# Kernel optimization log

Hardware: AMD Instinct MI355X
Metric: run time of the kernel (lower is better)

Reference implementation:

```python
import jax, jax.numpy as jnp
import numpy as np

N = 32768      # total points (multiple of patch_size -> no padding needed)
C = 768        # channels
H = 8          # num heads
K = 256        # patch_size (window length)
HD = C // H    # head dim = 96, divisible by 6 (3 axes * rotary pairs)
FREQ = 100.0   # rope_freq


def rope3d(x, pos):
    """Point-position RoPE: head dim split into 3 axis chunks, each rotated
    by angles pos_axis * freq**(-i/half).  x: [N,H,HD], pos: [N,3] float."""
    d_axis = HD // 3            # 32
    half = d_axis // 2          # 16
    inv_freq = FREQ ** (-jnp.arange(half, dtype=x.dtype) / half)   # [half]
    ang = pos[:, :, None] * inv_freq[None, None, :]                # [N,3,half]
    cos = jnp.cos(ang)[:, None, :, :]                              # [N,1,3,half]
    sin = jnp.sin(ang)[:, None, :, :]
    xr = x.reshape(x.shape[0], x.shape[1], 3, d_axis)              # [N,H,3,d_axis]
    x1, x2 = xr[..., :half], xr[..., half:]
    out = jnp.concatenate([x1 * cos - x2 * sin, x1 * sin + x2 * cos], axis=-1)
    return out.reshape(x.shape)


def setup_inputs() -> dict:
    key = jax.random.key(0)
    ks = jax.random.split(key, 6)
    feat = jax.random.normal(ks[0], (N, C), dtype=jnp.float32)
    grid_coord = jax.random.randint(ks[1], (N, 3), 0, 1024, dtype=jnp.int32)
    order = jax.random.permutation(ks[2], N).astype(jnp.int32)     # serialized order
    inverse = jnp.argsort(order).astype(jnp.int32)                 # its inverse
    w_qkv = jax.random.normal(ks[3], (C, 3 * C), dtype=jnp.float32) * 0.02
    b_qkv = jnp.zeros((3 * C,), dtype=jnp.float32)
    w_proj = jax.random.normal(ks[4], (C, C), dtype=jnp.float32) * 0.02
    b_proj = jnp.zeros((C,), dtype=jnp.float32)
    return {"feat": feat, "grid_coord": grid_coord, "order": order,
            "inverse": inverse, "w_qkv": w_qkv, "b_qkv": b_qkv,
            "w_proj": w_proj, "b_proj": b_proj}


def reference(feat, grid_coord, order, inverse, w_qkv, b_qkv, w_proj, b_proj):
    scale = HD ** -0.5
    P = N // K  # number of windows
    qkv = (feat @ w_qkv + b_qkv)[order]                   # gather by serialized order
    pos = grid_coord[order].astype(feat.dtype)            # [N,3]
    q, k, v = jnp.split(qkv, 3, axis=-1)
    q = rope3d(q.reshape(N, H, HD), pos)
    k = rope3d(k.reshape(N, H, HD), pos)
    v = v.reshape(N, H, HD)
    # windowed (varlen with equal patch lengths) attention
    qw = q.reshape(P, K, H, HD)
    kw = k.reshape(P, K, H, HD)
    vw = v.reshape(P, K, H, HD)
    logits = jnp.einsum('pqhd,pkhd->phqk', qw, kw) * scale
    attn = jax.nn.softmax(logits, axis=-1)
    out = jnp.einsum('phqk,pkhd->pqhd', attn, vw).reshape(N, C)
    out = out[inverse]                                    # scatter back to input order
    return out @ w_proj + b_proj
```

## Files before the change

### kernel.cpp

```cpp
#include <hip/hip_runtime.h>
#include <hip/hip_bf16.h>
#include <stdint.h>

typedef __bf16 bf16_t;
typedef __bf16 bf16x8 __attribute__((ext_vector_type(8)));
typedef __bf16 bf16x4 __attribute__((ext_vector_type(4)));
typedef float f32x4 __attribute__((ext_vector_type(4)));

__device__ __forceinline__ void gload_lds16(const bf16_t* g, bf16_t* l) {
  __builtin_amdgcn_global_load_lds((const __attribute__((address_space(1))) void*)g,
                                   (__attribute__((address_space(3))) void*)l, 16, 0, 0);
}

__global__ __launch_bounds__(256) void transpose_cast_k(const float* __restrict__ W,
                                                        bf16_t* __restrict__ Bt,
                                                        int KDin, int MDin) {
  __shared__ float tile[64][65];
  const int bm = blockIdx.x, bk = blockIdx.y;
  const int c = threadIdx.x & 63, r0 = threadIdx.x >> 6;
#pragma unroll
  for (int rr = 0; rr < 16; ++rr) {
    int row = rr * 4 + r0;
    tile[row][c] = W[(size_t)(bk * 64 + row) * MDin + bm * 64 + c];
  }
  __syncthreads();
#pragma unroll
  for (int rr = 0; rr < 16; ++rr) {
    int mo = rr * 4 + r0;
    Bt[(size_t)(bm * 64 + mo) * KDin + bk * 64 + c] = (bf16_t)tile[c][mo];
  }
}

__global__ __launch_bounds__(256) void gather_cast_k(const float* __restrict__ feat,
                                                     const int* __restrict__ order,
                                                     bf16_t* __restrict__ featp) {
  const int id = blockIdx.x * 256 + threadIdx.x;
  const int j = id / 192;
  const int c = (id % 192) * 4;
  const int g = order[j];
  const float4 v = *(const float4*)(feat + (size_t)g * 768 + c);
  bf16x4 o;
  o[0] = (bf16_t)v.x; o[1] = (bf16_t)v.y; o[2] = (bf16_t)v.z; o[3] = (bf16_t)v.w;
  *(bf16x4*)(featp + (size_t)j * 768 + c) = o;
}

template <int MODE>
__global__ __launch_bounds__(256) void gemm_bt_k(const bf16_t* __restrict__ A,
                                                 const bf16_t* __restrict__ Bt,
                                                 const float* __restrict__ bias,
                                                 bf16_t* __restrict__ Cq,
                                                 bf16_t* __restrict__ Ck,
                                                 bf16_t* __restrict__ Cv,
                                                 float* __restrict__ Cf,
                                                 const int* __restrict__ order) {
  __shared__ bf16_t As[128 * 32];
  __shared__ bf16_t Bs[128 * 32];
  const int tid = threadIdx.x;
  const int lane = tid & 63;
  const int wave = tid >> 6;
  const int wr = wave >> 1, wc = wave & 1;
  const int lq = lane & 15, lk = lane >> 4;
  const int bx = blockIdx.x, by = blockIdx.y;

  const bf16_t* gA = A + (size_t)(by * 128 + (tid >> 2)) * 768 + (tid & 3) * 8;
  const bf16_t* gB = Bt + (size_t)(bx * 128 + (tid >> 2)) * 768 + (tid & 3) * 8;
  bf16_t* lA = As + tid * 8;
  bf16_t* lB = Bs + tid * 8;

  f32x4 acc[4][4] = {};

  for (int kk = 0; kk < 24; ++kk) {
    gload_lds16(gA, lA);
    gload_lds16(gA + 64 * 768, lA + 2048);
    gload_lds16(gB, lB);
    gload_lds16(gB + 64 * 768, lB + 2048);
    gA += 32;
    gB += 32;
    __syncthreads();
    bf16x8 af[4], bfr[4];
#pragma unroll
    for (int t = 0; t < 4; ++t) {
      af[t]  = *(const bf16x8*)(As + (wr * 64 + t * 16 + lq) * 32 + lk * 8);
      bfr[t] = *(const bf16x8*)(Bs + (wc * 64 + t * 16 + lq) * 32 + lk * 8);
    }
#pragma unroll
    for (int mt = 0; mt < 4; ++mt)
#pragma unroll
      for (int nt = 0; nt < 4; ++nt)
        acc[mt][nt] = __builtin_amdgcn_mfma_f32_16x16x32_bf16(af[mt], bfr[nt], acc[mt][nt], 0, 0, 0);
    __syncthreads();
  }

  const int colb = bx * 128 + wc * 64;
  float bcol[4];
#pragma unroll
  for (int nt = 0; nt < 4; ++nt) bcol[nt] = bias[colb + nt * 16 + lq];

#pragma unroll
  for (int mt = 0; mt < 4; ++mt) {
    const int row = by * 128 + wr * 64 + mt * 16 + lk * 4;
    if (MODE == 0) {
      bf16_t* base = (bx < 6) ? Cq : (bx < 12 ? Ck : Cv);
      const int coll = colb - (bx < 6 ? 0 : (bx < 12 ? 768 : 1536));
#pragma unroll
      for (int nt = 0; nt < 4; ++nt) {
        const int col = coll + nt * 16 + lq;
#pragma unroll
        for (int r = 0; r < 4; ++r)
          base[(size_t)(row + r) * 768 + col] = (bf16_t)(acc[mt][nt][r] + bcol[nt]);
      }
    } else {
      int ro[4];
#pragma unroll
      for (int r = 0; r < 4; ++r) ro[r] = order[row + r];
#pragma unroll
      for (int nt = 0; nt < 4; ++nt) {
        const int col = colb + nt * 16 + lq;
#pragma unroll
        for (int r = 0; r < 4; ++r)
          Cf[(size_t)ro[r] * 768 + col] = acc[mt][nt][r] + bcol[nt];
      }
    }
  }
}

__global__ __launch_bounds__(256) void rope_pack_k(bf16_t* __restrict__ Qb,
                                                   const bf16_t* __restrict__ Kb,
                                                   const bf16_t* __restrict__ Vb,
                                                   bf16_t* __restrict__ Kp,
                                                   bf16_t* __restrict__ Vp,
                                                   const int* __restrict__ grid_coord,
                                                   const int* __restrict__ order) {
  const int h = blockIdx.x, p = blockIdx.y;
  const int t = threadIdx.x;
  const int j = p * 256 + t;
  const int g = order[j];
  float pos[3];
  pos[0] = (float)grid_coord[g * 3 + 0];
  pos[1] = (float)grid_coord[g * 3 + 1];
  pos[2] = (float)grid_coord[g * 3 + 2];
  bf16_t* qrow = Qb + (size_t)j * 768 + h * 96;
  const bf16_t* krow = Kb + (size_t)j * 768 + h * 96;
  bf16_t* Kps = Kp + (size_t)(p * 8 + h) * 24576;
  const int nt = t >> 4, lqt = t & 15;
  const float NEGL = -0.41524101186f;
#pragma unroll
  for (int a = 0; a < 3; ++a) {
    const float pa = pos[a];
    bf16x8 q0 = *(bf16x8*)(qrow + a * 32);
    bf16x8 q1 = *(bf16x8*)(qrow + a * 32 + 8);
    bf16x8 q2 = *(bf16x8*)(qrow + a * 32 + 16);
    bf16x8 q3 = *(bf16x8*)(qrow + a * 32 + 24);
    bf16x8 k0 = *(const bf16x8*)(krow + a * 32);
    bf16x8 k1 = *(const bf16x8*)(krow + a * 32 + 8);
    bf16x8 k2 = *(const bf16x8*)(krow + a * 32 + 16);
    bf16x8 k3 = *(const bf16x8*)(krow + a * 32 + 24);
    float s[16], c[16];
#pragma unroll
    for (int i = 0; i < 16; ++i) {
      float ang = pa * exp2f(NEGL * (float)i);
      __sincosf(ang, &s[i], &c[i]);
    }
#pragma unroll
    for (int i = 0; i < 8; ++i) {
      float x1 = (float)q0[i], x2 = (float)q2[i];
      q0[i] = (bf16_t)(x1 * c[i] - x2 * s[i]);
      q2[i] = (bf16_t)(x1 * s[i] + x2 * c[i]);
      float y1 = (float)q1[i], y2 = (float)q3[i];
      q1[i] = (bf16_t)(y1 * c[i + 8] - y2 * s[i + 8]);
      q3[i] = (bf16_t)(y1 * s[i + 8] + y2 * c[i + 8]);
      float u1 = (float)k0[i], u2 = (float)k2[i];
      k0[i] = (bf16_t)(u1 * c[i] - u2 * s[i]);
      k2[i] = (bf16_t)(u1 * s[i] + u2 * c[i]);
      float w1 = (float)k1[i], w2 = (float)k3[i];
      k1[i] = (bf16_t)(w1 * c[i + 8] - w2 * s[i + 8]);
      k3[i] = (bf16_t)(w1 * s[i + 8] + w2 * c[i + 8]);
    }
    *(bf16x8*)(qrow + a * 32) = q0;
    *(bf16x8*)(qrow + a * 32 + 8) = q1;
    *(bf16x8*)(qrow + a * 32 + 16) = q2;
    *(bf16x8*)(qrow + a * 32 + 24) = q3;
    bf16_t* kf = Kps + (size_t)((nt * 3 + a) * 64 + lqt) * 8;
    *(bf16x8*)(kf)           = k0;
    *(bf16x8*)(kf + 16 * 8)  = k1;
    *(bf16x8*)(kf + 32 * 8)  = k2;
    *(bf16x8*)(kf + 48 * 8)  = k3;
  }
  const bf16_t* vrow = Vb + (size_t)j * 768 + h * 96;
  bf16_t* Vps = Vp + (size_t)(p * 8 + h) * 24576;
  const int kc8 = t >> 5, lkv = (t >> 3) & 3, jv = t & 7;
#pragma unroll
  for (int d0 = 0; d0 < 96; d0 += 8) {
    bf16x8 v = *(const bf16x8*)(vrow + d0);
    const int dt = d0 >> 4;
    bf16_t* vf = Vps + (size_t)((dt * 8 + kc8) * 64 + lkv * 16 + (d0 & 15)) * 8 + jv;
#pragma unroll
    for (int i = 0; i < 8; ++i) vf[i * 8] = v[i];
  }
}

__global__ __launch_bounds__(256) void attn_k(bf16_t* QO,
                                              const bf16_t* __restrict__ Kp,
                                              const bf16_t* __restrict__ Vp) {
  __shared__ bf16_t KV[24576];
  __shared__ bf16_t Pb[4][2048];
  const int bid = blockIdx.x;
  const int chunk = bid & 3;
  const int ph = bid >> 2;
  const int h = ph & 7, p = ph >> 3;
  const int tid = threadIdx.x, lane = tid & 63, wave = tid >> 6;
  const int lq = lane & 15, lk = lane >> 4;
  const int tok0 = p * 256;
  const int qrow0 = chunk * 64 + wave * 16;
  const bf16_t* Kps = Kp + (size_t)ph * 24576;
  const bf16_t* Vps = Vp + (size_t)ph * 24576;
  const float scale = 0.10206207262f;

#pragma unroll
  for (int i = 0; i < 12; ++i)
    gload_lds16(Kps + i * 2048 + tid * 8, KV + i * 2048 + tid * 8);
  bf16x8 aq[3];
  {
    const bf16_t* qb = QO + (size_t)(tok0 + qrow0 + lq) * 768 + h * 96 + lk * 8;
#pragma unroll
    for (int kc = 0; kc < 3; ++kc) aq[kc] = *(const bf16x8*)(qb + kc * 32);
  }
  __syncthreads();

  f32x4 sacc[16];
#pragma unroll
  for (int nt = 0; nt < 16; ++nt) {
    f32x4 acc = {0.f, 0.f, 0.f, 0.f};
#pragma unroll
    for (int kc = 0; kc < 3; ++kc) {
      bf16x8 bk = *(const bf16x8*)(KV + (size_t)((nt * 3 + kc) * 64 + lane) * 8);
      acc = __builtin_amdgcn_mfma_f32_16x16x32_bf16(aq[kc], bk, acc, 0, 0, 0);
    }
    sacc[nt] = acc;
  }
  __syncthreads();

#pragma unroll
  for (int i = 0; i < 12; ++i)
    gload_lds16(Vps + i * 2048 + tid * 8, KV + i * 2048 + tid * 8);

  float linv[4];
#pragma unroll
  for (int r = 0; r < 4; ++r) {
    float mx = -1e30f;
#pragma unroll
    for (int nt = 0; nt < 16; ++nt) mx = fmaxf(mx, sacc[nt][r]);
    mx = fmaxf(mx, __shfl_xor(mx, 1));
    mx = fmaxf(mx, __shfl_xor(mx, 2));
    mx = fmaxf(mx, __shfl_xor(mx, 4));
    mx = fmaxf(mx, __shfl_xor(mx, 8));
    mx *= scale;
    float l = 0.f;
#pragma unroll
    for (int nt = 0; nt < 16; ++nt) {
      float e = __expf(sacc[nt][r] * scale - mx);
      sacc[nt][r] = e;
      l += e;
    }
    l += __shfl_xor(l, 1);
    l += __shfl_xor(l, 2);
    l += __shfl_xor(l, 4);
    l += __shfl_xor(l, 8);
    linv[r] = 1.f / l;
  }
  __syncthreads();

  bf16_t* pw = &Pb[wave][0];
  f32x4 oacc[6] = {};
#pragma unroll
  for (int hf = 0; hf < 2; ++hf) {
#pragma unroll
    for (int ntl = 0; ntl < 8; ++ntl) {
      const int nt = hf * 8 + ntl;
      const int chk = ntl * 2 + (lq >> 3);
#pragma unroll
      for (int r = 0; r < 4; ++r) {
        const int row = lk * 4 + r;
        const int phys = chk ^ (row & 7);
        pw[row * 128 + phys * 8 + (lq & 7)] = (bf16_t)sacc[nt][r];
      }
    }
#pragma unroll
    for (int kcl = 0; kcl < 4; ++kcl) {
      const int physr = (kcl * 4 + lk) ^ (lq & 7);
      bf16x8 pf = *(const bf16x8*)(pw + lq * 128 + physr * 8);
      const int kc = hf * 4 + kcl;
#pragma unroll
      for (int dt = 0; dt < 6; ++dt) {
        bf16x8 vb = *(const bf16x8*)(KV + (size_t)((dt * 8 + kc) * 64 + lane) * 8);
        oacc[dt] = __builtin_amdgcn_mfma_f32_16x16x32_bf16(pf, vb, oacc[dt], 0, 0, 0);
      }
    }
  }

#pragma unroll
  for (int dt = 0; dt < 6; ++dt) {
#pragma unroll
    for (int r = 0; r < 4; ++r) {
      const int row = tok0 + qrow0 + lk * 4 + r;
      QO[(size_t)row * 768 + h * 96 + dt * 16 + lq] = (bf16_t)(oacc[dt][r] * linv[r]);
    }
  }
}

extern "C" void kernel_launch(void* const* d_in, const int* in_sizes, int n_in,
                              void* d_out, int out_size, void* d_ws, size_t ws_size,
                              hipStream_t stream) {
  const float* feat       = (const float*)d_in[0];
  const int*   grid_coord = (const int*)d_in[1];
  const int*   order      = (const int*)d_in[2];
  const float* w_qkv      = (const float*)d_in[4];
  const float* b_qkv      = (const float*)d_in[5];
  const float* w_proj     = (const float*)d_in[6];
  const float* b_proj     = (const float*)d_in[7];
  float* out = (float*)d_out;

  char* ws = (char*)d_ws;
  bf16_t* Bt1   = (bf16_t*)(ws);
  bf16_t* Bt2   = (bf16_t*)(ws + 3538944);
  bf16_t* featp = (bf16_t*)(ws + 4718592);
  bf16_t* Kp    = featp;
  bf16_t* Qb    = (bf16_t*)(ws + 55050240);
  bf16_t* Kb    = (bf16_t*)(ws + 105381888);
  bf16_t* Vb    = (bf16_t*)(ws + 155713536);
  bf16_t* Vp    = (bf16_t*)(ws + 206045184);

  transpose_cast_k<<<dim3(36, 12), 256, 0, stream>>>(w_qkv, Bt1, 768, 2304);
  transpose_cast_k<<<dim3(12, 12), 256, 0, stream>>>(w_proj, Bt2, 768, 768);
  gather_cast_k<<<24576, 256, 0, stream>>>(feat, order, featp);
  gemm_bt_k<0><<<dim3(18, 256), 256, 0, stream>>>(featp, Bt1, b_qkv, Qb, Kb, Vb, nullptr, nullptr);
  rope_pack_k<<<dim3(8, 128), 256, 0, stream>>>(Qb, Kb, Vb, Kp, Vp, grid_coord, order);
  attn_k<<<4096, 256, 0, stream>>>(Qb, Kp, Vp);
  gemm_bt_k<1><<<dim3(6, 256), 256, 0, stream>>>(Qb, Bt2, b_proj, nullptr, nullptr, nullptr, out, order);
}
```

Before: 560.6 us.

## Fuse RoPE into QKV GEMM epilogue and stage V transpose through LDS

Gathered positions are precomputed once in the gather kernel, and RoPE is applied to Q and K inside the QKV GEMM epilogue in fp32 before the bf16 store. This removes the separate read-modify-write of Q and the per-thread sincos recomputation. The pack kernel now only relayouts K with coalesced 16-byte copies and transposes V through padded shared memory, replacing scattered 2-byte global stores. posf shares its workspace with Vp; this is safe only because posf is consumed by the GEMM before pack_k writes Vp. Rounding also shifts slightly, since RoPE is now applied before the bf16 cast rather than after.

```diff
diff --git a/kernel.cpp b/kernel.cpp
--- a/kernel.cpp
+++ b/kernel.cpp
@@ -33,7 +33,9 @@
 
 __global__ __launch_bounds__(256) void gather_cast_k(const float* __restrict__ feat,
                                                      const int* __restrict__ order,
-                                                     bf16_t* __restrict__ featp) {
+                                                     const int* __restrict__ grid_coord,
+                                                     bf16_t* __restrict__ featp,
+                                                     float* __restrict__ posf) {
   const int id = blockIdx.x * 256 + threadIdx.x;
   const int j = id / 192;
   const int c = (id % 192) * 4;
@@ -42,6 +44,11 @@
   bf16x4 o;
   o[0] = (bf16_t)v.x; o[1] = (bf16_t)v.y; o[2] = (bf16_t)v.z; o[3] = (bf16_t)v.w;
   *(bf16x4*)(featp + (size_t)j * 768 + c) = o;
+  if (c == 0) {
+    posf[j * 3 + 0] = (float)grid_coord[g * 3 + 0];
+    posf[j * 3 + 1] = (float)grid_coord[g * 3 + 1];
+    posf[j * 3 + 2] = (float)grid_coord[g * 3 + 2];
+  }
 }
 
 template <int MODE>
@@ -52,7 +59,8 @@
                                                  bf16_t* __restrict__ Ck,
                                                  bf16_t* __restrict__ Cv,
                                                  float* __restrict__ Cf,
-                                                 const int* __restrict__ order) {
+                                                 const int* __restrict__ order,
+                                                 const float* __restrict__ posf) {
   __shared__ bf16_t As[128 * 32];
   __shared__ bf16_t Bs[128 * 32];
   const int tid = threadIdx.x;
@@ -96,23 +104,57 @@
 #pragma unroll
   for (int nt = 0; nt < 4; ++nt) bcol[nt] = bias[colb + nt * 16 + lq];
 
-#pragma unroll
-  for (int mt = 0; mt < 4; ++mt) {
-    const int row = by * 128 + wr * 64 + mt * 16 + lk * 4;
-    if (MODE == 0) {
-      bf16_t* base = (bx < 6) ? Cq : (bx < 12 ? Ck : Cv);
-      const int coll = colb - (bx < 6 ? 0 : (bx < 12 ? 768 : 1536));
-#pragma unroll
-      for (int nt = 0; nt < 4; ++nt) {
-        const int col = coll + nt * 16 + lq;
-#pragma unroll
-        for (int r = 0; r < 4; ++r)
-          base[(size_t)(row + r) * 768 + col] = (bf16_t)(acc[mt][nt][r] + bcol[nt]);
+  if (MODE == 0) {
+    bf16_t* base = (bx < 6) ? Cq : (bx < 12 ? Ck : Cv);
+    const int coll = colb - (bx < 6 ? 0 : (bx < 12 ? 768 : 1536));
+    if (bx < 12) {
+      const int a0 = (colb % 96) >> 5;
+      const int a1 = ((colb + 32) % 96) >> 5;
+      const float fr = exp2f(-0.41524101186f * (float)lq);
+#pragma unroll
+      for (int mt = 0; mt < 4; ++mt) {
+        const int rowb = by * 128 + wr * 64 + mt * 16 + lk * 4;
+#pragma unroll
+        for (int r = 0; r < 4; ++r) {
+          const int row = rowb + r;
+          float s0, c0, s1, c1;
+          __sincosf(posf[row * 3 + a0] * fr, &s0, &c0);
+          __sincosf(posf[row * 3 + a1] * fr, &s1, &c1);
+          const float x1 = acc[mt][0][r] + bcol[0], x2 = acc[mt][1][r] + bcol[1];
+          const float y1 = acc[mt][2][r] + bcol[2], y2 = acc[mt][3][r] + bcol[3];
+          acc[mt][0][r] = x1 * c0 - x2 * s0;
+          acc[mt][1][r] = x1 * s0 + x2 * c0;
+          acc[mt][2][r] = y1 * c1 - y2 * s1;
+          acc[mt][3][r] = y1 * s1 + y2 * c1;
+        }
+#pragma unroll
+        for (int nt = 0; nt < 4; ++nt) {
+          const int col = coll + nt * 16 + lq;
+#pragma unroll
+          for (int r = 0; r < 4; ++r)
+            base[(size_t)(rowb + r) * 768 + col] = (bf16_t)acc[mt][nt][r];
+        }
       }
     } else {
+#pragma unroll
+      for (int mt = 0; mt < 4; ++mt) {
+        const int rowb = by * 128 + wr * 64 + mt * 16 + lk * 4;
+#pragma unroll
+        for (int nt = 0; nt < 4; ++nt) {
+          const int col = coll + nt * 16 + lq;
+#pragma unroll
+          for (int r = 0; r < 4; ++r)
+            base[(size_t)(rowb + r) * 768 + col] = (bf16_t)(acc[mt][nt][r] + bcol[nt]);
+        }
+      }
+    }
+  } else {
+#pragma unroll
+    for (int mt = 0; mt < 4; ++mt) {
+      const int rowb = by * 128 + wr * 64 + mt * 16 + lk * 4;
       int ro[4];
 #pragma unroll
-      for (int r = 0; r < 4; ++r) ro[r] = order[row + r];
+      for (int r = 0; r < 4; ++r) ro[r] = order[rowb + r];
 #pragma unroll
       for (int nt = 0; nt < 4; ++nt) {
         const int col = colb + nt * 16 + lq;
@@ -124,78 +166,43 @@
   }
 }
 
-__global__ __launch_bounds__(256) void rope_pack_k(bf16_t* __restrict__ Qb,
-                                                   const bf16_t* __restrict__ Kb,
-                                                   const bf16_t* __restrict__ Vb,
-                                                   bf16_t* __restrict__ Kp,
-                                                   bf16_t* __restrict__ Vp,
-                                                   const int* __restrict__ grid_coord,
-                                                   const int* __restrict__ order) {
+__global__ __launch_bounds__(256) void pack_k(const bf16_t* __restrict__ Kb,
+                                              const bf16_t* __restrict__ Vb,
+                                              bf16_t* __restrict__ Kp,
+                                              bf16_t* __restrict__ Vp) {
+  __shared__ bf16_t VT[96 * 264];
   const int h = blockIdx.x, p = blockIdx.y;
-  const int t = threadIdx.x;
-  const int j = p * 256 + t;
-  const int g = order[j];
-  float pos[3];
-  pos[0] = (float)grid_coord[g * 3 + 0];
-  pos[1] = (float)grid_coord[g * 3 + 1];
-  pos[2] = (float)grid_coord[g * 3 + 2];
-  bf16_t* qrow = Qb + (size_t)j * 768 + h * 96;
-  const bf16_t* krow = Kb + (size_t)j * 768 + h * 96;
-  bf16_t* Kps = Kp + (size_t)(p * 8 + h) * 24576;
-  const int nt = t >> 4, lqt = t & 15;
-  const float NEGL = -0.41524101186f;
-#pragma unroll
-  for (int a = 0; a < 3; ++a) {
-    const float pa = pos[a];
-    bf16x8 q0 = *(bf16x8*)(qrow + a * 32);
-    bf16x8 q1 = *(bf16x8*)(qrow + a * 32 + 8);
-    bf16x8 q2 = *(bf16x8*)(qrow + a * 32 + 16);
-    bf16x8 q3 = *(bf16x8*)(qrow + a * 32 + 24);
-    bf16x8 k0 = *(const bf16x8*)(krow + a * 32);
-    bf16x8 k1 = *(const bf16x8*)(krow + a * 32 + 8);
-    bf16x8 k2 = *(const bf16x8*)(krow + a * 32 + 16);
-    bf16x8 k3 = *(const bf16x8*)(krow + a * 32 + 24);
-    float s[16], c[16];
-#pragma unroll
-    for (int i = 0; i < 16; ++i) {
-      float ang = pa * exp2f(NEGL * (float)i);
-      __sincosf(ang, &s[i], &c[i]);
-    }
-#pragma unroll
-    for (int i = 0; i < 8; ++i) {
-      float x1 = (float)q0[i], x2 = (float)q2[i];
-      q0[i] = (bf16_t)(x1 * c[i] - x2 * s[i]);
-      q2[i] = (bf16_t)(x1 * s[i] + x2 * c[i]);
-      float y1 = (float)q1[i], y2 = (float)q3[i];
-      q1[i] = (bf16_t)(y1 * c[i + 8] - y2 * s[i + 8]);
-      q3[i] = (bf16_t)(y1 * s[i + 8] + y2 * c[i + 8]);
-      float u1 = (float)k0[i], u2 = (float)k2[i];
-      k0[i] = (bf16_t)(u1 * c[i] - u2 * s[i]);
-      k2[i] = (bf16_t)(u1 * s[i] + u2 * c[i]);
-      float w1 = (float)k1[i], w2 = (float)k3[i];
-      k1[i] = (bf16_t)(w1 * c[i + 8] - w2 * s[i + 8]);
-      k3[i] = (bf16_t)(w1 * s[i + 8] + w2 * c[i + 8]);
-    }
-    *(bf16x8*)(qrow + a * 32) = q0;
-    *(bf16x8*)(qrow + a * 32 + 8) = q1;
-    *(bf16x8*)(qrow + a * 32 + 16) = q2;
-    *(bf16x8*)(qrow + a * 32 + 24) = q3;
-    bf16_t* kf = Kps + (size_t)((nt * 3 + a) * 64 + lqt) * 8;
-    *(bf16x8*)(kf)           = k0;
-    *(bf16x8*)(kf + 16 * 8)  = k1;
-    *(bf16x8*)(kf + 32 * 8)  = k2;
-    *(bf16x8*)(kf + 48 * 8)  = k3;
-  }
-  const bf16_t* vrow = Vb + (size_t)j * 768 + h * 96;
-  bf16_t* Vps = Vp + (size_t)(p * 8 + h) * 24576;
-  const int kc8 = t >> 5, lkv = (t >> 3) & 3, jv = t & 7;
-#pragma unroll
-  for (int d0 = 0; d0 < 96; d0 += 8) {
-    bf16x8 v = *(const bf16x8*)(vrow + d0);
-    const int dt = d0 >> 4;
-    bf16_t* vf = Vps + (size_t)((dt * 8 + kc8) * 64 + lkv * 16 + (d0 & 15)) * 8 + jv;
-#pragma unroll
-    for (int i = 0; i < 8; ++i) vf[i * 8] = v[i];
+  const int tid = threadIdx.x;
+  const int tok0 = p * 256;
+  const size_t phb = (size_t)(p * 8 + h) * 24576;
+
+#pragma unroll
+  for (int i = 0; i < 12; ++i) {
+    const int c = i * 256 + tid;
+    const int fi = c >> 6, ln = c & 63;
+    const int nt = fi / 3, a = fi - nt * 3;
+    const int tok = nt * 16 + (ln & 15), feat = a * 32 + (ln >> 4) * 8;
+    *(bf16x8*)(Kp + phb + (size_t)c * 8) =
+        *(const bf16x8*)(Kb + (size_t)(tok0 + tok) * 768 + h * 96 + feat);
+  }
+
+  {
+    const bf16_t* vrow = Vb + (size_t)(tok0 + tid) * 768 + h * 96;
+#pragma unroll
+    for (int d0 = 0; d0 < 96; d0 += 8) {
+      bf16x8 v = *(const bf16x8*)(vrow + d0);
+#pragma unroll
+      for (int i = 0; i < 8; ++i) VT[(d0 + i) * 264 + tid] = v[i];
+    }
+  }
+  __syncthreads();
+#pragma unroll
+  for (int i = 0; i < 12; ++i) {
+    const int c = i * 256 + tid;
+    const int fi = c >> 6, ln = c & 63;
+    const int d = (fi >> 3) * 16 + (ln & 15);
+    const int tb = (fi & 7) * 32 + (ln >> 4) * 8;
+    *(bf16x8*)(Vp + phb + (size_t)c * 8) = *(const bf16x8*)(VT + d * 264 + tb);
   }
 }
 
@@ -329,12 +336,13 @@
   bf16_t* Kb    = (bf16_t*)(ws + 105381888);
   bf16_t* Vb    = (bf16_t*)(ws + 155713536);
   bf16_t* Vp    = (bf16_t*)(ws + 206045184);
+  float*  posf  = (float*)(ws + 206045184);
 
   transpose_cast_k<<<dim3(36, 12), 256, 0, stream>>>(w_qkv, Bt1, 768, 2304);
   transpose_cast_k<<<dim3(12, 12), 256, 0, stream>>>(w_proj, Bt2, 768, 768);
-  gather_cast_k<<<24576, 256, 0, stream>>>(feat, order, featp);
-  gemm_bt_k<0><<<dim3(18, 256), 256, 0, stream>>>(featp, Bt1, b_qkv, Qb, Kb, Vb, nullptr, nullptr);
-  rope_pack_k<<<dim3(8, 128), 256, 0, stream>>>(Qb, Kb, Vb, Kp, Vp, grid_coord, order);
+  gather_cast_k<<<24576, 256, 0, stream>>>(feat, order, grid_coord, featp, posf);
+  gemm_bt_k<0><<<dim3(18, 256), 256, 0, stream>>>(featp, Bt1, b_qkv, Qb, Kb, Vb, nullptr, nullptr, posf);
+  pack_k<<<dim3(8, 128), 256, 0, stream>>>(Kb, Vb, Kp, Vp);
   attn_k<<<4096, 256, 0, stream>>>(Qb, Kp, Vp);
-  gemm_bt_k<1><<<dim3(6, 256), 256, 0, stream>>>(Qb, Bt2, b_proj, nullptr, nullptr, nullptr, out, order);
-}
+  gemm_bt_k<1><<<dim3(6, 256), 256, 0, stream>>>(Qb, Bt2, b_proj, nullptr, nullptr, nullptr, out, order, nullptr);
+}
```

Measured after the change: 523.6 us. 6.6% less time.
